# Kernel tuning notes

Measured on AMD Instinct MI355X. Metric: run time of the kernel, lower is better.

## Reference

```python
import jax, jax.numpy as jnp
import numpy as np

T, B, E, H = 2048, 2, 1024, 16
D = E // H  # head_dim = 64

def setup_inputs() -> dict:
    key = jax.random.key(0)
    ks = jax.random.split(key, 9)
    s = 1.0 / np.sqrt(E)
    return {
        "query": jax.random.normal(ks[0], (T, B, E), dtype=jnp.float32),
        "Wq": jax.random.normal(ks[1], (E, E), dtype=jnp.float32) * s,
        "bq": jax.random.normal(ks[2], (E,), dtype=jnp.float32) * 0.02,
        "Wk": jax.random.normal(ks[3], (E, E), dtype=jnp.float32) * s,
        "bk": jax.random.normal(ks[4], (E,), dtype=jnp.float32) * 0.02,
        "Wv": jax.random.normal(ks[5], (E, E), dtype=jnp.float32) * s,
        "bv": jax.random.normal(ks[6], (E,), dtype=jnp.float32) * 0.02,
        "Wo": jax.random.normal(ks[7], (E, E), dtype=jnp.float32) * s,
        "bo": jax.random.normal(ks[8], (E,), dtype=jnp.float32) * 0.02,
    }

def reference(query, Wq, bq, Wk, bk, Wv, bv, Wo, bo):
    # query: [T, B, E] (fairseq Time x Batch x Channel layout)
    t, b, e = query.shape
    scaling = D ** -0.5
    q = (query @ Wq.T + bq) * scaling          # [T,B,E], scaled like fairseq
    k = query @ Wk.T + bk                      # self-attention: k,v from query
    v = query @ Wv.T + bv
    # split heads: [T,B,H,D]
    q = q.reshape(t, b, H, D)
    k = k.reshape(t, b, H, D)
    v = v.reshape(t, b, H, D)
    # attn weights: [B,H,T(tgt),S(src)]
    scores = jnp.einsum("tbhd,sbhd->bhts", q, k)
    probs = jax.nn.softmax(scores, axis=-1)
    # attend: [T,B,H,D] -> [T,B,E]
    ctx = jnp.einsum("bhts,sbhd->tbhd", probs, v).reshape(t, b, e)
    return ctx @ Wo.T + bo                     # [T,B,E]
```

## Files before the change

kernel.cpp:

```cpp
#include <hip/hip_runtime.h>
#include <hip/hip_bf16.h>
#include <math.h>

#define TT 2048
#define BB 2
#define EE 1024
#define HH 16
#define DD 64
#define RR (TT*BB)

typedef __bf16 bf16x8 __attribute__((ext_vector_type(8)));
typedef float  floatx4 __attribute__((ext_vector_type(4)));

__device__ __forceinline__ unsigned short f2b(float f) {
    union { float f; unsigned u; } x{f};
    return (unsigned short)((x.u + 0x7FFFu + ((x.u >> 16) & 1u)) >> 16);
}

__device__ __forceinline__ float exp2_fast(float x) {
    return __builtin_amdgcn_exp2f(x);
}

typedef const __attribute__((address_space(1))) unsigned int as1_u32;
typedef __attribute__((address_space(3))) unsigned int as3_u32;
__device__ __forceinline__ void gload16(const void* g, void* l) {
    __builtin_amdgcn_global_load_lds((as1_u32*)g, (as3_u32*)l, 16, 0, 0);
}

#define SCALE_Q 0.18033688011112042f

__global__ __launch_bounds__(256)
void pack_bf16(const float* __restrict__ x,  const float* __restrict__ wq,
               const float* __restrict__ wk, const float* __restrict__ wv,
               const float* __restrict__ wo, unsigned short* __restrict__ dst)
{
    const size_t e0 = ((size_t)blockIdx.x * 256 + threadIdx.x) * 8;
    const float* src;
    if (e0 < (size_t)4 * 1024 * 1024) {
        src = x + e0;
    } else {
        const int seg = (int)((e0 >> 20) - 4);
        const float* wsrc[4] = {wq, wk, wv, wo};
        src = wsrc[seg] + (e0 & ((1u << 20) - 1));
    }
    const float4 a = *(const float4*)src;
    const float4 b = *(const float4*)(src + 4);
    union { unsigned short u[8]; uint4 v; } p;
    p.u[0] = f2b(a.x); p.u[1] = f2b(a.y); p.u[2] = f2b(a.z); p.u[3] = f2b(a.w);
    p.u[4] = f2b(b.x); p.u[5] = f2b(b.y); p.u[6] = f2b(b.z); p.u[7] = f2b(b.w);
    *(uint4*)&dst[e0] = p.v;
}

template<int MODE>
__global__ __launch_bounds__(256)
void gemm_mfma(const unsigned short* __restrict__ A,
               const unsigned short* __restrict__ Bw,
               const float* __restrict__ b0, const float* __restrict__ b1,
               const float* __restrict__ b2,
               void* __restrict__ out0, void* __restrict__ out1,
               void* __restrict__ out2)
{
    __shared__ __align__(16) unsigned char smem[34816];
    unsigned short* ldsA = (unsigned short*)smem;
    unsigned short* ldsB = (unsigned short*)(smem + 8192);

    const int tid  = threadIdx.x;
    const int w    = tid >> 6;
    const int lane = tid & 63;
    const int quad = lane >> 4;
    const int l15  = lane & 15;
    const int wm   = w & 1;
    const int wn   = w >> 1;
    const int i0   = blockIdx.x * 128;
    const int j0   = blockIdx.y * 128;

    const unsigned short* ga[2];
    const unsigned short* gb[2];
    #pragma unroll
    for (int r = 0; r < 2; ++r) {
        const int slot = r * 256 + tid;
        const int row  = slot >> 2;
        const int gc   = (slot & 3) ^ ((row >> 1) & 3);
        ga[r] = A  + (size_t)(i0 + row) * EE + gc * 8;
        gb[r] = Bw + (size_t)(j0 + row) * EE + gc * 8;
    }

    floatx4 acc[4][4];
    #pragma unroll
    for (int mt = 0; mt < 4; ++mt)
        #pragma unroll
        for (int nt = 0; nt < 4; ++nt)
            acc[mt][nt] = (floatx4){0.f, 0.f, 0.f, 0.f};

    for (int kk = 0; kk < EE; kk += 32) {
        __syncthreads();
        gload16(ga[0] + kk, ldsA + (0 * 256 + w * 64) * 8);
        gload16(ga[1] + kk, ldsA + (1 * 256 + w * 64) * 8);
        gload16(gb[0] + kk, ldsB + (0 * 256 + w * 64) * 8);
        gload16(gb[1] + kk, ldsB + (1 * 256 + w * 64) * 8);
        __syncthreads();

        bf16x8 af[4], bfr[4];
        #pragma unroll
        for (int mt = 0; mt < 4; ++mt) {
            const int row = wm * 64 + mt * 16 + l15;
            af[mt] = __builtin_bit_cast(bf16x8,
                *(const uint4*)&ldsA[(row * 4 + (quad ^ ((row >> 1) & 3))) * 8]);
        }
        #pragma unroll
        for (int nt = 0; nt < 4; ++nt) {
            const int col = wn * 64 + nt * 16 + l15;
            bfr[nt] = __builtin_bit_cast(bf16x8,
                *(const uint4*)&ldsB[(col * 4 + (quad ^ ((col >> 1) & 3))) * 8]);
        }
        #pragma unroll
        for (int mt = 0; mt < 4; ++mt)
            #pragma unroll
            for (int nt = 0; nt < 4; ++nt)
                acc[mt][nt] = __builtin_amdgcn_mfma_f32_16x16x32_bf16(
                    af[mt], bfr[nt], acc[mt][nt], 0, 0, 0);
    }

    if (MODE == 1) {
        float* dst = (float*)out0;
        #pragma unroll
        for (int nt = 0; nt < 4; ++nt) {
            const int j = j0 + wn * 64 + nt * 16 + l15;
            const float bb = b0[j];
            #pragma unroll
            for (int mt = 0; mt < 4; ++mt) {
                const int i = i0 + wm * 64 + mt * 16 + quad * 4;
                #pragma unroll
                for (int r2 = 0; r2 < 4; ++r2)
                    dst[(size_t)(i + r2) * EE + j] = acc[mt][nt][r2] + bb;
            }
        }
    } else {
        const int which = j0 >> 10;
        const float scale = (which == 0) ? SCALE_Q : 1.0f;
        const float* bias = (which == 0) ? b0 : (which == 1) ? b1 : b2;
        if (which < 2) {
            unsigned short* dst = (unsigned short*)(which == 0 ? out0 : out1);
            #pragma unroll
            for (int nt = 0; nt < 4; ++nt) {
                const int j = (j0 & 1023) + wn * 64 + nt * 16 + l15;
                const int h = j >> 6, d = j & 63;
                const float bb = bias[j];
                #pragma unroll
                for (int mt = 0; mt < 4; ++mt) {
                    const int i = i0 + wm * 64 + mt * 16 + quad * 4;
                    #pragma unroll
                    for (int r2 = 0; r2 < 4; ++r2) {
                        const int ii = i + r2;
                        const int t = ii >> 1, b = ii & 1;
                        dst[((size_t)(b * HH + h) * TT + t) * DD + d] =
                            f2b((acc[mt][nt][r2] + bb) * scale);
                    }
                }
            }
        } else {
            __syncthreads();
            unsigned short* tr = (unsigned short*)smem + (size_t)w * 64 * 68;
            #pragma unroll
            for (int nt = 0; nt < 4; ++nt) {
                const int jl = nt * 16 + l15;
                const float bb = bias[(j0 & 1023) + wn * 64 + jl];
                #pragma unroll
                for (int mt = 0; mt < 4; ++mt) {
                    const int il0 = mt * 16 + quad * 4;
                    ushort4 h4;
                    h4.x = f2b(acc[mt][nt][0] + bb);
                    h4.y = f2b(acc[mt][nt][1] + bb);
                    h4.z = f2b(acc[mt][nt][2] + bb);
                    h4.w = f2b(acc[mt][nt][3] + bb);
                    *(ushort4*)&tr[jl * 68 + il0] = h4;
                }
            }
            __syncthreads();
            const int jg = (j0 & 1023) + wn * 64 + lane;
            const int h = jg >> 6, d = jg & 63;
            const int tb = (i0 + wm * 64) >> 1;
            const unsigned short* rp = tr + (size_t)lane * 68;
            unsigned short* dstV = (unsigned short*)out2;
            #pragma unroll
            for (int g = 0; g < 4; ++g) {
                union { unsigned short u[8]; uint4 v; } pe, po;
                #pragma unroll
                for (int k = 0; k < 8; ++k) {
                    pe.u[k] = rp[(g * 8 + k) * 2];
                    po.u[k] = rp[(g * 8 + k) * 2 + 1];
                }
                *(uint4*)&dstV[((size_t)(0 * HH + h) * DD + d) * TT + tb + g * 8] = pe.v;
                *(uint4*)&dstV[((size_t)(1 * HH + h) * DD + d) * TT + tb + g * 8] = po.v;
            }
        }
    }
}

__global__ __launch_bounds__(256)
void attn_mfma(const unsigned short* __restrict__ Q,
               const unsigned short* __restrict__ K,
               const unsigned short* __restrict__ Vt,
               unsigned short* __restrict__ ctx)
{
    __shared__ __align__(16) unsigned short ksm[64 * 64];
    __shared__ __align__(16) unsigned short vtm[64 * 64];
    __shared__ __align__(16) unsigned short ptm[4][16 * 64];

    const int tid  = threadIdx.x;
    const int w    = tid >> 6;
    const int lane = tid & 63;
    const int quad = lane >> 4;
    const int l15  = lane & 15;
    const int l7   = lane & 7;
    const int bh   = blockIdx.x;
    const int tt   = blockIdx.y;

    const unsigned short* Qh = Q  + (size_t)bh * TT * DD;
    const unsigned short* Kh = K  + (size_t)bh * TT * DD;
    const unsigned short* Vh = Vt + (size_t)bh * DD * TT;

    const int q0 = tt * 64 + w * 16;

    bf16x8 qf[2];
    #pragma unroll
    for (int kd = 0; kd < 2; ++kd)
        qf[kd] = __builtin_bit_cast(bf16x8,
            *(const uint4*)&Qh[(size_t)(q0 + l15) * DD + kd * 32 + quad * 8]);

    const unsigned short* kg[2];
    const unsigned short* vg[2];
    #pragma unroll
    for (int r = 0; r < 2; ++r) {
        const int slot = r * 256 + tid;
        const int row  = slot >> 3;
        const int gc   = (slot & 7) ^ (row & 7);
        kg[r] = Kh + (size_t)row * DD + gc * 8;
        vg[r] = Vh + (size_t)row * TT + gc * 8;
    }

    floatx4 cacc[4];
    #pragma unroll
    for (int dn = 0; dn < 4; ++dn)
        cacc[dn] = (floatx4){0.f, 0.f, 0.f, 0.f};
    float lsum = 0.f;

    for (int st = 0; st < TT / 64; ++st) {
        __syncthreads();
        gload16(kg[0] + (size_t)st * 64 * DD, ksm + ((size_t)0 * 256 + w * 64) * 8);
        gload16(kg[1] + (size_t)st * 64 * DD, ksm + ((size_t)1 * 256 + w * 64) * 8);
        gload16(vg[0] + (size_t)st * 64,      vtm + ((size_t)0 * 256 + w * 64) * 8);
        gload16(vg[1] + (size_t)st * 64,      vtm + ((size_t)1 * 256 + w * 64) * 8);
        __syncthreads();

        floatx4 S[4];
        #pragma unroll
        for (int mt = 0; mt < 4; ++mt) {
            const int row = mt * 16 + l15;
            const bf16x8 ka0 = __builtin_bit_cast(bf16x8,
                *(const uint4*)&ksm[(row * 8 + ((0 + quad) ^ l7)) * 8]);
            const bf16x8 ka1 = __builtin_bit_cast(bf16x8,
                *(const uint4*)&ksm[(row * 8 + ((4 + quad) ^ l7)) * 8]);
            floatx4 s = (floatx4){0.f, 0.f, 0.f, 0.f};
            s = __builtin_amdgcn_mfma_f32_16x16x32_bf16(ka0, qf[0], s, 0, 0, 0);
            s = __builtin_amdgcn_mfma_f32_16x16x32_bf16(ka1, qf[1], s, 0, 0, 0);
            S[mt] = s;
        }

        float rs = 0.f;
        #pragma unroll
        for (int mt = 0; mt < 4; ++mt) {
            const float p0 = exp2_fast(S[mt][0]);
            const float p1 = exp2_fast(S[mt][1]);
            const float p2 = exp2_fast(S[mt][2]);
            const float p3 = exp2_fast(S[mt][3]);
            rs += (p0 + p1) + (p2 + p3);
            union { __hip_bfloat162 h2[2]; uint2 u; } pk;
            pk.h2[0] = __float22bfloat162_rn(make_float2(p0, p1));
            pk.h2[1] = __float22bfloat162_rn(make_float2(p2, p3));
            const int cc = mt * 2 + (quad >> 1);
            *(uint2*)&ptm[w][(l15 * 8 + (cc ^ l7)) * 8 + ((quad & 1) << 2)] = pk.u;
        }
        rs += __shfl_xor(rs, 16);
        rs += __shfl_xor(rs, 32);
        lsum += rs;

        const bf16x8 pa0 = __builtin_bit_cast(bf16x8,
            *(const uint4*)&ptm[w][(l15 * 8 + ((0 + quad) ^ l7)) * 8]);
        const bf16x8 pa1 = __builtin_bit_cast(bf16x8,
            *(const uint4*)&ptm[w][(l15 * 8 + ((4 + quad) ^ l7)) * 8]);

        #pragma unroll
        for (int dn = 0; dn < 4; ++dn) {
            const int row = dn * 16 + l15;
            const bf16x8 vb0 = __builtin_bit_cast(bf16x8,
                *(const uint4*)&vtm[(row * 8 + ((0 + quad) ^ l7)) * 8]);
            const bf16x8 vb1 = __builtin_bit_cast(bf16x8,
                *(const uint4*)&vtm[(row * 8 + ((4 + quad) ^ l7)) * 8]);
            cacc[dn] = __builtin_amdgcn_mfma_f32_16x16x32_bf16(pa0, vb0, cacc[dn], 0, 0, 0);
            cacc[dn] = __builtin_amdgcn_mfma_f32_16x16x32_bf16(pa1, vb1, cacc[dn], 0, 0, 0);
        }
    }

    const int b = bh / HH, hh = bh % HH;
    const float linv = 1.0f / lsum;
    float lj[4];
    #pragma unroll
    for (int j = 0; j < 4; ++j)
        lj[j] = __shfl(linv, (quad << 2) + j);
    #pragma unroll
    for (int dn = 0; dn < 4; ++dn) {
        const int e = hh * 64 + dn * 16 + l15;
        #pragma unroll
        for (int j = 0; j < 4; ++j) {
            const int t = q0 + quad * 4 + j;
            ctx[(size_t)(t * BB + b) * EE + e] = f2b(cacc[dn][j] * lj[j]);
        }
    }
}

extern "C" void kernel_launch(void* const* d_in, const int* in_sizes, int n_in,
                              void* d_out, int out_size, void* d_ws, size_t ws_size,
                              hipStream_t stream)
{
    const float* x  = (const float*)d_in[0];
    const float* Wq = (const float*)d_in[1];
    const float* bq = (const float*)d_in[2];
    const float* Wk = (const float*)d_in[3];
    const float* bk = (const float*)d_in[4];
    const float* Wv = (const float*)d_in[5];
    const float* bv = (const float*)d_in[6];
    const float* Wo = (const float*)d_in[7];
    const float* bo = (const float*)d_in[8];
    float* out = (float*)d_out;

    const size_t M1 = 1024 * 1024;
    unsigned short* base = (unsigned short*)d_ws;
    unsigned short* xb   = base;
    unsigned short* wqkv = base + 4 * M1;
    unsigned short* wob  = base + 7 * M1;
    unsigned short* qb   = base + 8 * M1;
    unsigned short* kb   = base + 12 * M1;
    unsigned short* vtb  = base + 16 * M1;
    unsigned short* cb   = base + 20 * M1;

    dim3 blk(256);

    pack_bf16<<<dim3(4096), blk, 0, stream>>>(x, Wq, Wk, Wv, Wo, base);

    gemm_mfma<0><<<dim3(RR / 128, 3072 / 128), blk, 0, stream>>>(
        xb, wqkv, bq, bk, bv, qb, kb, vtb);

    attn_mfma<<<dim3(BB * HH, TT / 64), blk, 0, stream>>>(qb, kb, vtb, cb);

    gemm_mfma<1><<<dim3(RR / 128, EE / 128), blk, 0, stream>>>(
        cb, wob, bo, nullptr, nullptr, out, nullptr, nullptr);
}
```

Baseline: 211.0 us.

## Split attention over two key halves with combine pass, shrink GEMM tiles

The attention kernel now splits the key/value sequence into two halves along a third grid dimension. Each half writes unnormalized bf16 context and its row sums, and a new combine kernel adds the halves and normalizes. The GEMM kernels use smaller tiles (128x64 for the QKV projection, 64x64 for the output projection) to launch more blocks, and the V-transpose epilogue is rewritten to match. This aims to raise parallelism and CU occupancy. In exchange it adds an extra kernel, extra partial-buffer memory traffic, reduced per-block data reuse, and an extra bf16 rounding of the partial context.

Measured after the change: 210.2 us. No clear change (-0.4%).

```diff
diff --git a/kernel.cpp b/kernel.cpp
--- a/kernel.cpp
+++ b/kernel.cpp
@@ -16,6 +16,12 @@
     union { float f; unsigned u; } x{f};
     return (unsigned short)((x.u + 0x7FFFu + ((x.u >> 16) & 1u)) >> 16);
 }
+__device__ __forceinline__ float b2f_lo(unsigned u) {
+    union { unsigned u; float f; } x{u << 16}; return x.f;
+}
+__device__ __forceinline__ float b2f_hi(unsigned u) {
+    union { unsigned u; float f; } x{u & 0xffff0000u}; return x.f;
+}
 
 __device__ __forceinline__ float exp2_fast(float x) {
     return __builtin_amdgcn_exp2f(x);
@@ -32,23 +38,29 @@
 __global__ __launch_bounds__(256)
 void pack_bf16(const float* __restrict__ x,  const float* __restrict__ wq,
                const float* __restrict__ wk, const float* __restrict__ wv,
-               const float* __restrict__ wo, unsigned short* __restrict__ dst)
+               const float* __restrict__ wo, unsigned short* __restrict__ base,
+               unsigned short* __restrict__ wob)
 {
+    const size_t M4 = (size_t)4 << 20, M7 = (size_t)7 << 20;
     const size_t e0 = ((size_t)blockIdx.x * 256 + threadIdx.x) * 8;
     const float* src;
-    if (e0 < (size_t)4 * 1024 * 1024) {
-        src = x + e0;
+    unsigned short* dst;
+    if (e0 < M4) {
+        src = x + e0; dst = base + e0;
+    } else if (e0 < M7) {
+        const int seg = (int)((e0 >> 20) - 4);
+        const float* wsrc[3] = {wq, wk, wv};
+        src = wsrc[seg] + (e0 & ((1u << 20) - 1));
+        dst = base + e0;
     } else {
-        const int seg = (int)((e0 >> 20) - 4);
-        const float* wsrc[4] = {wq, wk, wv, wo};
-        src = wsrc[seg] + (e0 & ((1u << 20) - 1));
+        src = wo + (e0 - M7); dst = wob + (e0 - M7);
     }
     const float4 a = *(const float4*)src;
     const float4 b = *(const float4*)(src + 4);
     union { unsigned short u[8]; uint4 v; } p;
     p.u[0] = f2b(a.x); p.u[1] = f2b(a.y); p.u[2] = f2b(a.z); p.u[3] = f2b(a.w);
     p.u[4] = f2b(b.x); p.u[5] = f2b(b.y); p.u[6] = f2b(b.z); p.u[7] = f2b(b.w);
-    *(uint4*)&dst[e0] = p.v;
+    *(uint4*)dst = p.v;
 }
 
 template<int MODE>
@@ -60,9 +72,16 @@
                void* __restrict__ out0, void* __restrict__ out1,
                void* __restrict__ out2)
 {
-    __shared__ __align__(16) unsigned char smem[34816];
+    constexpr int BM = (MODE == 0) ? 128 : 64;
+    constexpr int BN = 64;
+    constexpr int MT = BM / 32;
+    constexpr int NT = BN / 32;
+    constexpr int RA = BM / 64;
+    constexpr int RB = BN / 64;
+    constexpr int SMEM = (MODE == 0) ? 17408 : 8192;
+    __shared__ __align__(16) unsigned char smem[SMEM];
     unsigned short* ldsA = (unsigned short*)smem;
-    unsigned short* ldsB = (unsigned short*)(smem + 8192);
+    unsigned short* ldsB = (unsigned short*)(smem + BM * 64);
 
     const int tid  = threadIdx.x;
     const int w    = tid >> 6;
@@ -71,52 +90,60 @@
     const int l15  = lane & 15;
     const int wm   = w & 1;
     const int wn   = w >> 1;
-    const int i0   = blockIdx.x * 128;
-    const int j0   = blockIdx.y * 128;
-
-    const unsigned short* ga[2];
-    const unsigned short* gb[2];
-    #pragma unroll
-    for (int r = 0; r < 2; ++r) {
+    const int i0   = blockIdx.x * BM;
+    const int j0   = blockIdx.y * BN;
+
+    const unsigned short* ga[RA];
+    const unsigned short* gb[RB];
+    #pragma unroll
+    for (int r = 0; r < RA; ++r) {
         const int slot = r * 256 + tid;
         const int row  = slot >> 2;
         const int gc   = (slot & 3) ^ ((row >> 1) & 3);
-        ga[r] = A  + (size_t)(i0 + row) * EE + gc * 8;
+        ga[r] = A + (size_t)(i0 + row) * EE + gc * 8;
+    }
+    #pragma unroll
+    for (int r = 0; r < RB; ++r) {
+        const int slot = r * 256 + tid;
+        const int row  = slot >> 2;
+        const int gc   = (slot & 3) ^ ((row >> 1) & 3);
         gb[r] = Bw + (size_t)(j0 + row) * EE + gc * 8;
     }
 
-    floatx4 acc[4][4];
-    #pragma unroll
-    for (int mt = 0; mt < 4; ++mt)
-        #pragma unroll
-        for (int nt = 0; nt < 4; ++nt)
+    floatx4 acc[MT][NT];
+    #pragma unroll
+    for (int mt = 0; mt < MT; ++mt)
+        #pragma unroll
+        for (int nt = 0; nt < NT; ++nt)
             acc[mt][nt] = (floatx4){0.f, 0.f, 0.f, 0.f};
 
     for (int kk = 0; kk < EE; kk += 32) {
         __syncthreads();
-        gload16(ga[0] + kk, ldsA + (0 * 256 + w * 64) * 8);
-        gload16(ga[1] + kk, ldsA + (1 * 256 + w * 64) * 8);
-        gload16(gb[0] + kk, ldsB + (0 * 256 + w * 64) * 8);
-        gload16(gb[1] + kk, ldsB + (1 * 256 + w * 64) * 8);
+        #pragma unroll
+        for (int r = 0; r < RA; ++r)
+            gload16(ga[r] + kk, ldsA + (r * 256 + w * 64) * 8);
+        #pragma unroll
+        for (int r = 0; r < RB; ++r)
+            gload16(gb[r] + kk, ldsB + (r * 256 + w * 64) * 8);
         __syncthreads();
 
-        bf16x8 af[4], bfr[4];
-        #pragma unroll
-        for (int mt = 0; mt < 4; ++mt) {
-            const int row = wm * 64 + mt * 16 + l15;
+        bf16x8 af[MT], bfr[NT];
+        #pragma unroll
+        for (int mt = 0; mt < MT; ++mt) {
+            const int row = wm * (BM / 2) + mt * 16 + l15;
             af[mt] = __builtin_bit_cast(bf16x8,
                 *(const uint4*)&ldsA[(row * 4 + (quad ^ ((row >> 1) & 3))) * 8]);
         }
         #pragma unroll
-        for (int nt = 0; nt < 4; ++nt) {
-            const int col = wn * 64 + nt * 16 + l15;
+        for (int nt = 0; nt < NT; ++nt) {
+            const int col = wn * (BN / 2) + nt * 16 + l15;
             bfr[nt] = __builtin_bit_cast(bf16x8,
                 *(const uint4*)&ldsB[(col * 4 + (quad ^ ((col >> 1) & 3))) * 8]);
         }
         #pragma unroll
-        for (int mt = 0; mt < 4; ++mt)
-            #pragma unroll
-            for (int nt = 0; nt < 4; ++nt)
+        for (int mt = 0; mt < MT; ++mt)
+            #pragma unroll
+            for (int nt = 0; nt < NT; ++nt)
                 acc[mt][nt] = __builtin_amdgcn_mfma_f32_16x16x32_bf16(
                     af[mt], bfr[nt], acc[mt][nt], 0, 0, 0);
     }
@@ -124,12 +151,12 @@
     if (MODE == 1) {
         float* dst = (float*)out0;
         #pragma unroll
-        for (int nt = 0; nt < 4; ++nt) {
-            const int j = j0 + wn * 64 + nt * 16 + l15;
+        for (int nt = 0; nt < NT; ++nt) {
+            const int j = j0 + wn * 32 + nt * 16 + l15;
             const float bb = b0[j];
             #pragma unroll
-            for (int mt = 0; mt < 4; ++mt) {
-                const int i = i0 + wm * 64 + mt * 16 + quad * 4;
+            for (int mt = 0; mt < MT; ++mt) {
+                const int i = i0 + wm * 32 + mt * 16 + quad * 4;
                 #pragma unroll
                 for (int r2 = 0; r2 < 4; ++r2)
                     dst[(size_t)(i + r2) * EE + j] = acc[mt][nt][r2] + bb;
@@ -137,17 +164,18 @@
         }
     } else {
         const int which = j0 >> 10;
+        const int jh = j0 & 1023;
+        const int h = jh >> 6;
         const float scale = (which == 0) ? SCALE_Q : 1.0f;
         const float* bias = (which == 0) ? b0 : (which == 1) ? b1 : b2;
         if (which < 2) {
             unsigned short* dst = (unsigned short*)(which == 0 ? out0 : out1);
             #pragma unroll
-            for (int nt = 0; nt < 4; ++nt) {
-                const int j = (j0 & 1023) + wn * 64 + nt * 16 + l15;
-                const int h = j >> 6, d = j & 63;
-                const float bb = bias[j];
+            for (int nt = 0; nt < NT; ++nt) {
+                const int d = wn * 32 + nt * 16 + l15;
+                const float bb = bias[jh + d];
                 #pragma unroll
-                for (int mt = 0; mt < 4; ++mt) {
+                for (int mt = 0; mt < MT; ++mt) {
                     const int i = i0 + wm * 64 + mt * 16 + quad * 4;
                     #pragma unroll
                     for (int r2 = 0; r2 < 4; ++r2) {
@@ -160,38 +188,40 @@
             }
         } else {
             __syncthreads();
-            unsigned short* tr = (unsigned short*)smem + (size_t)w * 64 * 68;
-            #pragma unroll
-            for (int nt = 0; nt < 4; ++nt) {
-                const int jl = nt * 16 + l15;
-                const float bb = bias[(j0 & 1023) + wn * 64 + jl];
+            unsigned short* tr = (unsigned short*)smem + (size_t)w * 32 * 68;
+            #pragma unroll
+            for (int nt = 0; nt < NT; ++nt) {
+                const int dl = nt * 16 + l15;
+                const float bb = bias[jh + wn * 32 + dl];
                 #pragma unroll
-                for (int mt = 0; mt < 4; ++mt) {
+                for (int mt = 0; mt < MT; ++mt) {
                     const int il0 = mt * 16 + quad * 4;
                     ushort4 h4;
                     h4.x = f2b(acc[mt][nt][0] + bb);
                     h4.y = f2b(acc[mt][nt][1] + bb);
                     h4.z = f2b(acc[mt][nt][2] + bb);
                     h4.w = f2b(acc[mt][nt][3] + bb);
-                    *(ushort4*)&tr[jl * 68 + il0] = h4;
+                    *(ushort4*)&tr[dl * 68 + il0] = h4;
                 }
             }
             __syncthreads();
-            const int jg = (j0 & 1023) + wn * 64 + lane;
-            const int h = jg >> 6, d = jg & 63;
-            const int tb = (i0 + wm * 64) >> 1;
-            const unsigned short* rp = tr + (size_t)lane * 68;
+            const int dl2 = lane & 31;
+            const int ih  = lane >> 5;
+            const int d   = wn * 32 + dl2;
+            const int t0  = (i0 + wm * 64 + ih * 32) >> 1;
+            const unsigned* rp32 = (const unsigned*)(tr + dl2 * 68 + ih * 32);
+            union { unsigned short u[16]; uint4 v[2]; } pe, po;
+            #pragma unroll
+            for (int k = 0; k < 16; ++k) {
+                const unsigned u = rp32[k];
+                pe.u[k] = (unsigned short)(u & 0xffffu);
+                po.u[k] = (unsigned short)(u >> 16);
+            }
             unsigned short* dstV = (unsigned short*)out2;
             #pragma unroll
-            for (int g = 0; g < 4; ++g) {
-                union { unsigned short u[8]; uint4 v; } pe, po;
-                #pragma unroll
-                for (int k = 0; k < 8; ++k) {
-                    pe.u[k] = rp[(g * 8 + k) * 2];
-                    po.u[k] = rp[(g * 8 + k) * 2 + 1];
-                }
-                *(uint4*)&dstV[((size_t)(0 * HH + h) * DD + d) * TT + tb + g * 8] = pe.v;
-                *(uint4*)&dstV[((size_t)(1 * HH + h) * DD + d) * TT + tb + g * 8] = po.v;
+            for (int g = 0; g < 2; ++g) {
+                *(uint4*)&dstV[((size_t)(0 * HH + h) * DD + d) * TT + t0 + g * 8] = pe.v[g];
+                *(uint4*)&dstV[((size_t)(1 * HH + h) * DD + d) * TT + t0 + g * 8] = po.v[g];
             }
         }
     }
@@ -201,7 +231,8 @@
 void attn_mfma(const unsigned short* __restrict__ Q,
                const unsigned short* __restrict__ K,
                const unsigned short* __restrict__ Vt,
-               unsigned short* __restrict__ ctx)
+               unsigned short* __restrict__ cpart,
+               float* __restrict__ lsumbuf)
 {
     __shared__ __align__(16) unsigned short ksm[64 * 64];
     __shared__ __align__(16) unsigned short vtm[64 * 64];
@@ -215,6 +246,7 @@
     const int l7   = lane & 7;
     const int bh   = blockIdx.x;
     const int tt   = blockIdx.y;
+    const int half = blockIdx.z;
 
     const unsigned short* Qh = Q  + (size_t)bh * TT * DD;
     const unsigned short* Kh = K  + (size_t)bh * TT * DD;
@@ -245,7 +277,7 @@
         cacc[dn] = (floatx4){0.f, 0.f, 0.f, 0.f};
     float lsum = 0.f;
 
-    for (int st = 0; st < TT / 64; ++st) {
+    for (int st = half * 16; st < half * 16 + 16; ++st) {
         __syncthreads();
         gload16(kg[0] + (size_t)st * 64 * DD, ksm + ((size_t)0 * 256 + w * 64) * 8);
         gload16(kg[1] + (size_t)st * 64 * DD, ksm + ((size_t)1 * 256 + w * 64) * 8);
@@ -303,20 +335,47 @@
     }
 
     const int b = bh / HH, hh = bh % HH;
-    const float linv = 1.0f / lsum;
-    float lj[4];
-    #pragma unroll
-    for (int j = 0; j < 4; ++j)
-        lj[j] = __shfl(linv, (quad << 2) + j);
+    unsigned short* cp = cpart + (size_t)half * RR * EE;
     #pragma unroll
     for (int dn = 0; dn < 4; ++dn) {
         const int e = hh * 64 + dn * 16 + l15;
         #pragma unroll
         for (int j = 0; j < 4; ++j) {
             const int t = q0 + quad * 4 + j;
-            ctx[(size_t)(t * BB + b) * EE + e] = f2b(cacc[dn][j] * lj[j]);
-        }
-    }
+            cp[(size_t)(t * BB + b) * EE + e] = f2b(cacc[dn][j]);
+        }
+    }
+    if (quad == 0)
+        lsumbuf[(half * BB * HH + bh) * TT + q0 + l15] = lsum;
+}
+
+__global__ __launch_bounds__(256)
+void combine(const unsigned short* __restrict__ cpart,
+             const float* __restrict__ lsumbuf,
+             unsigned short* __restrict__ cb)
+{
+    const int gid = blockIdx.x * 256 + threadIdx.x;
+    const int e0 = (gid & 127) * 8;
+    const int r  = gid >> 7;
+    const int t = r >> 1, b = r & 1;
+    const int h = e0 >> 6;
+    const int bh = b * HH + h;
+    const float inv = 1.0f /
+        (lsumbuf[bh * TT + t] + lsumbuf[(BB * HH + bh) * TT + t]);
+    const uint4 c0 = *(const uint4*)&cpart[(size_t)r * EE + e0];
+    const uint4 c1 = *(const uint4*)&cpart[(size_t)RR * EE + (size_t)r * EE + e0];
+    const unsigned u0[4] = {c0.x, c0.y, c0.z, c0.w};
+    const unsigned u1[4] = {c1.x, c1.y, c1.z, c1.w};
+    union { unsigned u[4]; uint4 v; } o;
+    #pragma unroll
+    for (int k = 0; k < 4; ++k) {
+        const float lo = (b2f_lo(u0[k]) + b2f_lo(u1[k])) * inv;
+        const float hi = (b2f_hi(u0[k]) + b2f_hi(u1[k])) * inv;
+        union { __hip_bfloat162 h2; unsigned u; } pk;
+        pk.h2 = __float22bfloat162_rn(make_float2(lo, hi));
+        o.u[k] = pk.u;
+    }
+    *(uint4*)&cb[(size_t)r * EE + e0] = o.v;
 }
 
 extern "C" void kernel_launch(void* const* d_in, const int* in_sizes, int n_in,
@@ -334,25 +393,29 @@
     const float* bo = (const float*)d_in[8];
     float* out = (float*)d_out;
 
-    const size_t M1 = 1024 * 1024;
+    const size_t M1 = (size_t)1 << 20;
     unsigned short* base = (unsigned short*)d_ws;
-    unsigned short* xb   = base;
-    unsigned short* wqkv = base + 4 * M1;
-    unsigned short* wob  = base + 7 * M1;
-    unsigned short* qb   = base + 8 * M1;
-    unsigned short* kb   = base + 12 * M1;
-    unsigned short* vtb  = base + 16 * M1;
-    unsigned short* cb   = base + 20 * M1;
+    unsigned short* xb    = base;
+    unsigned short* wqkv  = base + 4 * M1;
+    unsigned short* cpart = base;
+    unsigned short* qb    = base + 8 * M1;
+    unsigned short* kb    = base + 12 * M1;
+    unsigned short* vtb   = base + 16 * M1;
+    unsigned short* cb    = base + 20 * M1;
+    unsigned short* wob   = base + 24 * M1;
+    float*          lsum  = (float*)(base + 25 * M1);
 
     dim3 blk(256);
 
-    pack_bf16<<<dim3(4096), blk, 0, stream>>>(x, Wq, Wk, Wv, Wo, base);
-
-    gemm_mfma<0><<<dim3(RR / 128, 3072 / 128), blk, 0, stream>>>(
+    pack_bf16<<<dim3(4096), blk, 0, stream>>>(x, Wq, Wk, Wv, Wo, base, wob);
+
+    gemm_mfma<0><<<dim3(RR / 128, 3072 / 64), blk, 0, stream>>>(
         xb, wqkv, bq, bk, bv, qb, kb, vtb);
 
-    attn_mfma<<<dim3(BB * HH, TT / 64), blk, 0, stream>>>(qb, kb, vtb, cb);
-
-    gemm_mfma<1><<<dim3(RR / 128, EE / 128), blk, 0, stream>>>(
+    attn_mfma<<<dim3(BB * HH, TT / 64, 2), blk, 0, stream>>>(qb, kb, vtb, cpart, lsum);
+
+    combine<<<dim3(RR * EE / 8 / 256), blk, 0, stream>>>(cpart, lsum, cb);
+
+    gemm_mfma<1><<<dim3(RR / 64, EE / 64), blk, 0, stream>>>(
         cb, wob, bo, nullptr, nullptr, out, nullptr, nullptr);
 }
```

## Keep attention probabilities in registers, double queries per warp, shrink output GEMM tiles

Applied to the files above, without the earlier changes.

The attention kernel now has each warp process 32 query rows instead of 16, reusing every K/V fragment loaded from LDS for two query tiles. It also permutes the K rows so that the exp'd score fragments can be packed straight into the A operand of the PV MFMA, removing the per-warp LDS round trip for probabilities. The output projection GEMM switches to 64x64 tiles to launch more blocks on the small problem. Risks are higher register pressure, with launch bounds now requesting 4 blocks per CU, and correctness depending on the new row permutation and swizzle matching the MFMA layout.

Measured after the change: 197.7 us. 1.07x faster.

```diff
diff --git a/kernel.cpp b/kernel.cpp
--- a/kernel.cpp
+++ b/kernel.cpp
@@ -28,6 +28,10 @@
 }
 
 #define SCALE_Q 0.18033688011112042f
+
+__device__ __forceinline__ int swz(int r) {
+    return (r & 7) ^ (((r >> 3) & 3) << 1);
+}
 
 __global__ __launch_bounds__(256)
 void pack_bf16(const float* __restrict__ x,  const float* __restrict__ wq,
@@ -60,9 +64,16 @@
                void* __restrict__ out0, void* __restrict__ out1,
                void* __restrict__ out2)
 {
-    __shared__ __align__(16) unsigned char smem[34816];
+    constexpr int BM = (MODE == 0) ? 128 : 64;
+    constexpr int BN = (MODE == 0) ? 128 : 64;
+    constexpr int MT = BM / 32;
+    constexpr int NT = BN / 32;
+    constexpr int RA = BM / 64;
+    constexpr int RB = BN / 64;
+    constexpr int SMEM = (MODE == 0) ? 34816 : 8192;
+    __shared__ __align__(16) unsigned char smem[SMEM];
     unsigned short* ldsA = (unsigned short*)smem;
-    unsigned short* ldsB = (unsigned short*)(smem + 8192);
+    unsigned short* ldsB = (unsigned short*)(smem + BM * 64);
 
     const int tid  = threadIdx.x;
     const int w    = tid >> 6;
@@ -71,52 +82,60 @@
     const int l15  = lane & 15;
     const int wm   = w & 1;
     const int wn   = w >> 1;
-    const int i0   = blockIdx.x * 128;
-    const int j0   = blockIdx.y * 128;
-
-    const unsigned short* ga[2];
-    const unsigned short* gb[2];
-    #pragma unroll
-    for (int r = 0; r < 2; ++r) {
+    const int i0   = blockIdx.x * BM;
+    const int j0   = blockIdx.y * BN;
+
+    const unsigned short* ga[RA];
+    const unsigned short* gb[RB];
+    #pragma unroll
+    for (int r = 0; r < RA; ++r) {
         const int slot = r * 256 + tid;
         const int row  = slot >> 2;
         const int gc   = (slot & 3) ^ ((row >> 1) & 3);
-        ga[r] = A  + (size_t)(i0 + row) * EE + gc * 8;
+        ga[r] = A + (size_t)(i0 + row) * EE + gc * 8;
+    }
+    #pragma unroll
+    for (int r = 0; r < RB; ++r) {
+        const int slot = r * 256 + tid;
+        const int row  = slot >> 2;
+        const int gc   = (slot & 3) ^ ((row >> 1) & 3);
         gb[r] = Bw + (size_t)(j0 + row) * EE + gc * 8;
     }
 
-    floatx4 acc[4][4];
-    #pragma unroll
-    for (int mt = 0; mt < 4; ++mt)
-        #pragma unroll
-        for (int nt = 0; nt < 4; ++nt)
+    floatx4 acc[MT][NT];
+    #pragma unroll
+    for (int mt = 0; mt < MT; ++mt)
+        #pragma unroll
+        for (int nt = 0; nt < NT; ++nt)
             acc[mt][nt] = (floatx4){0.f, 0.f, 0.f, 0.f};
 
     for (int kk = 0; kk < EE; kk += 32) {
         __syncthreads();
-        gload16(ga[0] + kk, ldsA + (0 * 256 + w * 64) * 8);
-        gload16(ga[1] + kk, ldsA + (1 * 256 + w * 64) * 8);
-        gload16(gb[0] + kk, ldsB + (0 * 256 + w * 64) * 8);
-        gload16(gb[1] + kk, ldsB + (1 * 256 + w * 64) * 8);
+        #pragma unroll
+        for (int r = 0; r < RA; ++r)
+            gload16(ga[r] + kk, ldsA + (r * 256 + w * 64) * 8);
+        #pragma unroll
+        for (int r = 0; r < RB; ++r)
+            gload16(gb[r] + kk, ldsB + (r * 256 + w * 64) * 8);
         __syncthreads();
 
-        bf16x8 af[4], bfr[4];
-        #pragma unroll
-        for (int mt = 0; mt < 4; ++mt) {
-            const int row = wm * 64 + mt * 16 + l15;
+        bf16x8 af[MT], bfr[NT];
+        #pragma unroll
+        for (int mt = 0; mt < MT; ++mt) {
+            const int row = wm * (BM / 2) + mt * 16 + l15;
             af[mt] = __builtin_bit_cast(bf16x8,
                 *(const uint4*)&ldsA[(row * 4 + (quad ^ ((row >> 1) & 3))) * 8]);
         }
         #pragma unroll
-        for (int nt = 0; nt < 4; ++nt) {
-            const int col = wn * 64 + nt * 16 + l15;
+        for (int nt = 0; nt < NT; ++nt) {
+            const int col = wn * (BN / 2) + nt * 16 + l15;
             bfr[nt] = __builtin_bit_cast(bf16x8,
                 *(const uint4*)&ldsB[(col * 4 + (quad ^ ((col >> 1) & 3))) * 8]);
         }
         #pragma unroll
-        for (int mt = 0; mt < 4; ++mt)
-            #pragma unroll
-            for (int nt = 0; nt < 4; ++nt)
+        for (int mt = 0; mt < MT; ++mt)
+            #pragma unroll
+            for (int nt = 0; nt < NT; ++nt)
                 acc[mt][nt] = __builtin_amdgcn_mfma_f32_16x16x32_bf16(
                     af[mt], bfr[nt], acc[mt][nt], 0, 0, 0);
     }
@@ -124,12 +143,12 @@
     if (MODE == 1) {
         float* dst = (float*)out0;
         #pragma unroll
-        for (int nt = 0; nt < 4; ++nt) {
-            const int j = j0 + wn * 64 + nt * 16 + l15;
+        for (int nt = 0; nt < NT; ++nt) {
+            const int j = j0 + wn * (BN / 2) + nt * 16 + l15;
             const float bb = b0[j];
             #pragma unroll
-            for (int mt = 0; mt < 4; ++mt) {
-                const int i = i0 + wm * 64 + mt * 16 + quad * 4;
+            for (int mt = 0; mt < MT; ++mt) {
+                const int i = i0 + wm * (BM / 2) + mt * 16 + quad * 4;
                 #pragma unroll
                 for (int r2 = 0; r2 < 4; ++r2)
                     dst[(size_t)(i + r2) * EE + j] = acc[mt][nt][r2] + bb;
@@ -142,12 +161,12 @@
         if (which < 2) {
             unsigned short* dst = (unsigned short*)(which == 0 ? out0 : out1);
             #pragma unroll
-            for (int nt = 0; nt < 4; ++nt) {
+            for (int nt = 0; nt < NT; ++nt) {
                 const int j = (j0 & 1023) + wn * 64 + nt * 16 + l15;
                 const int h = j >> 6, d = j & 63;
                 const float bb = bias[j];
                 #pragma unroll
-                for (int mt = 0; mt < 4; ++mt) {
+                for (int mt = 0; mt < MT; ++mt) {
                     const int i = i0 + wm * 64 + mt * 16 + quad * 4;
                     #pragma unroll
                     for (int r2 = 0; r2 < 4; ++r2) {
@@ -162,11 +181,11 @@
             __syncthreads();
             unsigned short* tr = (unsigned short*)smem + (size_t)w * 64 * 68;
             #pragma unroll
-            for (int nt = 0; nt < 4; ++nt) {
+            for (int nt = 0; nt < NT; ++nt) {
                 const int jl = nt * 16 + l15;
                 const float bb = bias[(j0 & 1023) + wn * 64 + jl];
                 #pragma unroll
-                for (int mt = 0; mt < 4; ++mt) {
+                for (int mt = 0; mt < MT; ++mt) {
                     const int il0 = mt * 16 + quad * 4;
                     ushort4 h4;
                     h4.x = f2b(acc[mt][nt][0] + bb);
@@ -197,7 +216,7 @@
     }
 }
 
-__global__ __launch_bounds__(256)
+__global__ __launch_bounds__(256, 4)
 void attn_mfma(const unsigned short* __restrict__ Q,
                const unsigned short* __restrict__ K,
                const unsigned short* __restrict__ Vt,
@@ -205,14 +224,12 @@
 {
     __shared__ __align__(16) unsigned short ksm[64 * 64];
     __shared__ __align__(16) unsigned short vtm[64 * 64];
-    __shared__ __align__(16) unsigned short ptm[4][16 * 64];
 
     const int tid  = threadIdx.x;
     const int w    = tid >> 6;
     const int lane = tid & 63;
     const int quad = lane >> 4;
     const int l15  = lane & 15;
-    const int l7   = lane & 7;
     const int bh   = blockIdx.x;
     const int tt   = blockIdx.y;
 
@@ -220,13 +237,15 @@
     const unsigned short* Kh = K  + (size_t)bh * TT * DD;
     const unsigned short* Vh = Vt + (size_t)bh * DD * TT;
 
-    const int q0 = tt * 64 + w * 16;
-
-    bf16x8 qf[2];
-    #pragma unroll
-    for (int kd = 0; kd < 2; ++kd)
-        qf[kd] = __builtin_bit_cast(bf16x8,
-            *(const uint4*)&Qh[(size_t)(q0 + l15) * DD + kd * 32 + quad * 8]);
+    const int q0w = tt * 128 + w * 32;
+
+    bf16x8 qf[2][2];
+    #pragma unroll
+    for (int qn = 0; qn < 2; ++qn)
+        #pragma unroll
+        for (int kd = 0; kd < 2; ++kd)
+            qf[qn][kd] = __builtin_bit_cast(bf16x8,
+                *(const uint4*)&Qh[(size_t)(q0w + qn * 16 + l15) * DD + kd * 32 + quad * 8]);
 
     const unsigned short* kg[2];
     const unsigned short* vg[2];
@@ -234,87 +253,110 @@
     for (int r = 0; r < 2; ++r) {
         const int slot = r * 256 + tid;
         const int row  = slot >> 3;
-        const int gc   = (slot & 7) ^ (row & 7);
+        const int gc   = (slot & 7) ^ swz(row);
         kg[r] = Kh + (size_t)row * DD + gc * 8;
         vg[r] = Vh + (size_t)row * TT + gc * 8;
     }
 
-    floatx4 cacc[4];
+    int ofsKA[4][2], ofsVB[4][2];
+    #pragma unroll
+    for (int mt = 0; mt < 4; ++mt) {
+        const int row = ((mt >> 1) << 5) + ((l15 >> 2) << 3) + ((mt & 1) << 2) + (l15 & 3);
+        #pragma unroll
+        for (int kd = 0; kd < 2; ++kd)
+            ofsKA[mt][kd] = row * 64 + (((kd * 4 + quad) ^ swz(row)) << 3);
+    }
+    #pragma unroll
+    for (int dn = 0; dn < 4; ++dn) {
+        const int row = dn * 16 + l15;
+        #pragma unroll
+        for (int ks = 0; ks < 2; ++ks)
+            ofsVB[dn][ks] = row * 64 + (((ks * 4 + quad) ^ swz(row)) << 3);
+    }
+
+    floatx4 cacc[4][2];
     #pragma unroll
     for (int dn = 0; dn < 4; ++dn)
-        cacc[dn] = (floatx4){0.f, 0.f, 0.f, 0.f};
-    float lsum = 0.f;
+        #pragma unroll
+        for (int qn = 0; qn < 2; ++qn)
+            cacc[dn][qn] = (floatx4){0.f, 0.f, 0.f, 0.f};
+    float rs[2] = {0.f, 0.f};
 
     for (int st = 0; st < TT / 64; ++st) {
         __syncthreads();
-        gload16(kg[0] + (size_t)st * 64 * DD, ksm + ((size_t)0 * 256 + w * 64) * 8);
-        gload16(kg[1] + (size_t)st * 64 * DD, ksm + ((size_t)1 * 256 + w * 64) * 8);
-        gload16(vg[0] + (size_t)st * 64,      vtm + ((size_t)0 * 256 + w * 64) * 8);
-        gload16(vg[1] + (size_t)st * 64,      vtm + ((size_t)1 * 256 + w * 64) * 8);
+        gload16(kg[0] + (size_t)st * 64 * DD, ksm + (size_t)(0 * 256 + w * 64) * 8);
+        gload16(kg[1] + (size_t)st * 64 * DD, ksm + (size_t)(1 * 256 + w * 64) * 8);
+        gload16(vg[0] + (size_t)st * 64,      vtm + (size_t)(0 * 256 + w * 64) * 8);
+        gload16(vg[1] + (size_t)st * 64,      vtm + (size_t)(1 * 256 + w * 64) * 8);
         __syncthreads();
 
-        floatx4 S[4];
+        uint2 pk[4][2];
         #pragma unroll
         for (int mt = 0; mt < 4; ++mt) {
-            const int row = mt * 16 + l15;
-            const bf16x8 ka0 = __builtin_bit_cast(bf16x8,
-                *(const uint4*)&ksm[(row * 8 + ((0 + quad) ^ l7)) * 8]);
-            const bf16x8 ka1 = __builtin_bit_cast(bf16x8,
-                *(const uint4*)&ksm[(row * 8 + ((4 + quad) ^ l7)) * 8]);
-            floatx4 s = (floatx4){0.f, 0.f, 0.f, 0.f};
-            s = __builtin_amdgcn_mfma_f32_16x16x32_bf16(ka0, qf[0], s, 0, 0, 0);
-            s = __builtin_amdgcn_mfma_f32_16x16x32_bf16(ka1, qf[1], s, 0, 0, 0);
-            S[mt] = s;
-        }
-
-        float rs = 0.f;
-        #pragma unroll
-        for (int mt = 0; mt < 4; ++mt) {
-            const float p0 = exp2_fast(S[mt][0]);
-            const float p1 = exp2_fast(S[mt][1]);
-            const float p2 = exp2_fast(S[mt][2]);
-            const float p3 = exp2_fast(S[mt][3]);
-            rs += (p0 + p1) + (p2 + p3);
-            union { __hip_bfloat162 h2[2]; uint2 u; } pk;
-            pk.h2[0] = __float22bfloat162_rn(make_float2(p0, p1));
-            pk.h2[1] = __float22bfloat162_rn(make_float2(p2, p3));
-            const int cc = mt * 2 + (quad >> 1);
-            *(uint2*)&ptm[w][(l15 * 8 + (cc ^ l7)) * 8 + ((quad & 1) << 2)] = pk.u;
-        }
-        rs += __shfl_xor(rs, 16);
-        rs += __shfl_xor(rs, 32);
-        lsum += rs;
-
-        const bf16x8 pa0 = __builtin_bit_cast(bf16x8,
-            *(const uint4*)&ptm[w][(l15 * 8 + ((0 + quad) ^ l7)) * 8]);
-        const bf16x8 pa1 = __builtin_bit_cast(bf16x8,
-            *(const uint4*)&ptm[w][(l15 * 8 + ((4 + quad) ^ l7)) * 8]);
+            const bf16x8 ka0 = __builtin_bit_cast(bf16x8, *(const uint4*)&ksm[ofsKA[mt][0]]);
+            const bf16x8 ka1 = __builtin_bit_cast(bf16x8, *(const uint4*)&ksm[ofsKA[mt][1]]);
+            #pragma unroll
+            for (int qn = 0; qn < 2; ++qn) {
+                floatx4 s = (floatx4){0.f, 0.f, 0.f, 0.f};
+                s = __builtin_amdgcn_mfma_f32_16x16x32_bf16(ka0, qf[qn][0], s, 0, 0, 0);
+                s = __builtin_amdgcn_mfma_f32_16x16x32_bf16(ka1, qf[qn][1], s, 0, 0, 0);
+                const float p0 = exp2_fast(s[0]);
+                const float p1 = exp2_fast(s[1]);
+                const float p2 = exp2_fast(s[2]);
+                const float p3 = exp2_fast(s[3]);
+                rs[qn] += (p0 + p1) + (p2 + p3);
+                union { __hip_bfloat162 h2[2]; uint2 u; } c;
+                c.h2[0] = __float22bfloat162_rn(make_float2(p0, p1));
+                c.h2[1] = __float22bfloat162_rn(make_float2(p2, p3));
+                pk[mt][qn] = c.u;
+            }
+        }
+
+        bf16x8 pa[2][2];
+        #pragma unroll
+        for (int qn = 0; qn < 2; ++qn) {
+            union { uint2 d[2]; uint4 v; } a0, a1;
+            a0.d[0] = pk[0][qn]; a0.d[1] = pk[1][qn];
+            a1.d[0] = pk[2][qn]; a1.d[1] = pk[3][qn];
+            pa[qn][0] = __builtin_bit_cast(bf16x8, a0.v);
+            pa[qn][1] = __builtin_bit_cast(bf16x8, a1.v);
+        }
 
         #pragma unroll
         for (int dn = 0; dn < 4; ++dn) {
-            const int row = dn * 16 + l15;
-            const bf16x8 vb0 = __builtin_bit_cast(bf16x8,
-                *(const uint4*)&vtm[(row * 8 + ((0 + quad) ^ l7)) * 8]);
-            const bf16x8 vb1 = __builtin_bit_cast(bf16x8,
-                *(const uint4*)&vtm[(row * 8 + ((4 + quad) ^ l7)) * 8]);
-            cacc[dn] = __builtin_amdgcn_mfma_f32_16x16x32_bf16(pa0, vb0, cacc[dn], 0, 0, 0);
-            cacc[dn] = __builtin_amdgcn_mfma_f32_16x16x32_bf16(pa1, vb1, cacc[dn], 0, 0, 0);
+            const bf16x8 vb0 = __builtin_bit_cast(bf16x8, *(const uint4*)&vtm[ofsVB[dn][0]]);
+            const bf16x8 vb1 = __builtin_bit_cast(bf16x8, *(const uint4*)&vtm[ofsVB[dn][1]]);
+            #pragma unroll
+            for (int qn = 0; qn < 2; ++qn) {
+                cacc[dn][qn] = __builtin_amdgcn_mfma_f32_16x16x32_bf16(pa[qn][0], vb0, cacc[dn][qn], 0, 0, 0);
+                cacc[dn][qn] = __builtin_amdgcn_mfma_f32_16x16x32_bf16(pa[qn][1], vb1, cacc[dn][qn], 0, 0, 0);
+            }
         }
     }
 
     const int b = bh / HH, hh = bh % HH;
-    const float linv = 1.0f / lsum;
-    float lj[4];
-    #pragma unroll
-    for (int j = 0; j < 4; ++j)
-        lj[j] = __shfl(linv, (quad << 2) + j);
-    #pragma unroll
-    for (int dn = 0; dn < 4; ++dn) {
-        const int e = hh * 64 + dn * 16 + l15;
-        #pragma unroll
-        for (int j = 0; j < 4; ++j) {
-            const int t = q0 + quad * 4 + j;
-            ctx[(size_t)(t * BB + b) * EE + e] = f2b(cacc[dn][j] * lj[j]);
+    float linv[2];
+    #pragma unroll
+    for (int qn = 0; qn < 2; ++qn) {
+        float t = rs[qn];
+        t += __shfl_xor(t, 16);
+        t += __shfl_xor(t, 32);
+        linv[qn] = 1.0f / t;
+    }
+    #pragma unroll
+    for (int qn = 0; qn < 2; ++qn) {
+        float lj[4];
+        #pragma unroll
+        for (int j = 0; j < 4; ++j)
+            lj[j] = __shfl(linv[qn], quad * 4 + j);
+        #pragma unroll
+        for (int dn = 0; dn < 4; ++dn) {
+            const int e = hh * 64 + dn * 16 + l15;
+            #pragma unroll
+            for (int j = 0; j < 4; ++j) {
+                const int t = q0w + qn * 16 + quad * 4 + j;
+                ctx[(size_t)(t * BB + b) * EE + e] = f2b(cacc[dn][qn][j] * lj[j]);
+            }
         }
     }
 }
@@ -351,8 +393,8 @@
     gemm_mfma<0><<<dim3(RR / 128, 3072 / 128), blk, 0, stream>>>(
         xb, wqkv, bq, bk, bv, qb, kb, vtb);
 
-    attn_mfma<<<dim3(BB * HH, TT / 64), blk, 0, stream>>>(qb, kb, vtb, cb);
-
-    gemm_mfma<1><<<dim3(RR / 128, EE / 128), blk, 0, stream>>>(
+    attn_mfma<<<dim3(BB * HH, TT / 128), blk, 0, stream>>>(qb, kb, vtb, cb);
+
+    gemm_mfma<1><<<dim3(RR / 64, EE / 64), blk, 0, stream>>>(
         cb, wob, bo, nullptr, nullptr, out, nullptr, nullptr);
 }
```
